# Kernel tuning notes

Measured on AMD Instinct MI355X. Metric: run time of the kernel, lower is better.

## Reference

```python
import jax, jax.numpy as jnp
import numpy as np

DIM = 512
HEADS = 8
HEAD_DIM = DIM // HEADS
HIDDEN = 4 * DIM
EPS = 1e-5


def _ln(x, g, b):
    mu = jnp.mean(x, axis=-1, keepdims=True)
    var = jnp.mean((x - mu) ** 2, axis=-1, keepdims=True)
    return (x - mu) * jax.lax.rsqrt(var + EPS) * g + b


def setup_inputs() -> dict:
    key = jax.random.key(0)
    ks = jax.random.split(key, 12)
    s = lambda fan: 1.0 / np.sqrt(fan)
    return {
        "x": jax.random.normal(ks[0], (2, 4096, DIM), jnp.float32),
        "ln1_g": jnp.ones((DIM,), jnp.float32),
        "ln1_b": jnp.zeros((DIM,), jnp.float32),
        "ln2_g": jnp.ones((DIM,), jnp.float32),
        "ln2_b": jnp.zeros((DIM,), jnp.float32),
        "qkv_w": jax.random.normal(ks[1], (3 * DIM, DIM), jnp.float32) * s(DIM),
        "qkv_b": jnp.zeros((3 * DIM,), jnp.float32),
        "proj_w": jax.random.normal(ks[2], (DIM, DIM), jnp.float32) * s(DIM),
        "proj_b": jnp.zeros((DIM,), jnp.float32),
        "fc1_w": jax.random.normal(ks[3], (HIDDEN, DIM), jnp.float32) * s(DIM),
        "fc1_b": jnp.zeros((HIDDEN,), jnp.float32),
        "fc2_w": jax.random.normal(ks[4], (DIM, HIDDEN), jnp.float32) * s(HIDDEN),
        "fc2_b": jnp.zeros((DIM,), jnp.float32),
    }


def reference(x, ln1_g, ln1_b, ln2_g, ln2_b, qkv_w, qkv_b, proj_w, proj_b,
              fc1_w, fc1_b, fc2_w, fc2_b):
    B, N, C = x.shape
    # --- attention (pre-norm) ---
    h = _ln(x, ln1_g, ln1_b)
    qkv = h @ qkv_w.T + qkv_b                      # [B,N,3C]
    qkv = qkv.reshape(B, N, 3, HEADS, HEAD_DIM)
    q, k, v = (jnp.moveaxis(qkv, 2, 0)[i].transpose(0, 2, 1, 3) for i in range(3))  # [B,H,N,D]
    scale = HEAD_DIM ** -0.5
    attn = jax.nn.softmax(jnp.einsum('bhnd,bhmd->bhnm', q, k) * scale, axis=-1)
    out = jnp.einsum('bhnm,bhmd->bhnd', attn, v)   # [B,H,N,D]
    out = out.transpose(0, 2, 1, 3).reshape(B, N, C)
    x = x + out @ proj_w.T + proj_b
    # --- MLP (pre-norm) ---
    h = _ln(x, ln2_g, ln2_b)
    h = jax.nn.gelu(h @ fc1_w.T + fc1_b, approximate=False)
    return x + h @ fc2_w.T + fc2_b
```

## Files before the change

kernel.cpp:

```cpp
#include <hip/hip_runtime.h>
#include <hip/hip_bf16.h>
#include <string.h>

using bf16 = __hip_bfloat16;
typedef __attribute__((ext_vector_type(8))) short short8;
typedef __attribute__((ext_vector_type(4))) float f32x4;
typedef __attribute__((ext_vector_type(16))) float f32x16;

#define GAS __attribute__((address_space(1)))
#define LAS __attribute__((address_space(3)))

__device__ __forceinline__ void gld_lds16(const void* g, void* l) {
  __builtin_amdgcn_global_load_lds((const GAS void*)g, (LAS void*)l, 16, 0, 0);
}

__device__ __forceinline__ unsigned short f2bfu(float f) {
  bf16 h = __float2bfloat16(f);
  return *reinterpret_cast<unsigned short*>(&h);
}

__device__ __forceinline__ unsigned pack_bf16x2(float lo, float hi) {
  __hip_bfloat162 v = __float22bfloat162_rn(make_float2(lo, hi));
  unsigned u;
  __builtin_memcpy(&u, &v, 4);
  return u;
}

__global__ __launch_bounds__(256) void cvt_all(const float* __restrict__ w0, bf16* __restrict__ o0,
                                               const float* __restrict__ w1, bf16* __restrict__ o1,
                                               const float* __restrict__ w2, bf16* __restrict__ o2,
                                               const float* __restrict__ w3, bf16* __restrict__ o3) {
  int i = blockIdx.x * 256 + threadIdx.x;
  const float* src; bf16* dst; int off;
  if (i < 196608)      { src = w0; dst = o0; off = i; }
  else if (i < 262144) { src = w1; dst = o1; off = i - 196608; }
  else if (i < 524288) { src = w2; dst = o2; off = i - 262144; }
  else                 { src = w3; dst = o3; off = i - 524288; }
  float4 v = reinterpret_cast<const float4*>(src)[off];
  ushort4 o;
  o.x = f2bfu(v.x); o.y = f2bfu(v.y); o.z = f2bfu(v.z); o.w = f2bfu(v.w);
  reinterpret_cast<ushort4*>(dst)[off] = o;
}

__global__ __launch_bounds__(256) void ln_kernel(const float* __restrict__ x,
                                                 const float* __restrict__ g,
                                                 const float* __restrict__ b,
                                                 bf16* __restrict__ out) {
  const int row = blockIdx.x * 4 + (threadIdx.x >> 6);
  const int lane = threadIdx.x & 63;
  const float4* xr = reinterpret_cast<const float4*>(x + (size_t)row * 512);
  float4 v0 = xr[lane], v1 = xr[64 + lane];
  float s  = v0.x + v0.y + v0.z + v0.w + v1.x + v1.y + v1.z + v1.w;
  float s2 = v0.x*v0.x + v0.y*v0.y + v0.z*v0.z + v0.w*v0.w
           + v1.x*v1.x + v1.y*v1.y + v1.z*v1.z + v1.w*v1.w;
  #pragma unroll
  for (int d = 1; d < 64; d <<= 1) { s += __shfl_xor(s, d); s2 += __shfl_xor(s2, d); }
  const float mu = s * (1.0f / 512.0f);
  const float var = s2 * (1.0f / 512.0f) - mu * mu;
  const float rstd = rsqrtf(var + 1e-5f);
  const float4* g4 = reinterpret_cast<const float4*>(g);
  const float4* b4 = reinterpret_cast<const float4*>(b);
  float4 ga = g4[lane], gb = g4[64 + lane], ba = b4[lane], bb = b4[64 + lane];
  ushort4 o0, o1;
  o0.x = f2bfu((v0.x - mu) * rstd * ga.x + ba.x);
  o0.y = f2bfu((v0.y - mu) * rstd * ga.y + ba.y);
  o0.z = f2bfu((v0.z - mu) * rstd * ga.z + ba.z);
  o0.w = f2bfu((v0.w - mu) * rstd * ga.w + ba.w);
  o1.x = f2bfu((v1.x - mu) * rstd * gb.x + bb.x);
  o1.y = f2bfu((v1.y - mu) * rstd * gb.y + bb.y);
  o1.z = f2bfu((v1.z - mu) * rstd * gb.z + bb.z);
  o1.w = f2bfu((v1.w - mu) * rstd * gb.w + bb.w);
  ushort4* orow = reinterpret_cast<ushort4*>(out + (size_t)row * 512);
  orow[lane] = o0;
  orow[64 + lane] = o1;
}

template <int EPI>
__global__ __launch_bounds__(256) void gemm_bt(const bf16* __restrict__ A,
                                               const bf16* __restrict__ B,
                                               const float* __restrict__ bias,
                                               const float* __restrict__ resid,
                                               void* __restrict__ Cv,
                                               int M, int N, int K) {
  __shared__ bf16 As[128 * 32];
  __shared__ bf16 Bs[128 * 32];
  const int tid = threadIdx.x;
  const int lane = tid & 63, wid = tid >> 6;
  const int lr = lane & 15, lg = lane >> 4;
  const int row0 = blockIdx.x * 128, col0 = blockIdx.y * 128;
  const int wr = (wid >> 1) * 64, wc = (wid & 1) * 64;
  f32x4 acc[4][4] = {};
  const int r1 = tid >> 2,          c1 = (tid & 3) * 8;
  const int r2 = (256 + tid) >> 2,  c2 = ((256 + tid) & 3) * 8;
  for (int kt = 0; kt < K; kt += 32) {
    __syncthreads();
    gld_lds16(A + (size_t)(row0 + r1) * K + kt + c1, As + tid * 8);
    gld_lds16(A + (size_t)(row0 + r2) * K + kt + c2, As + (256 + tid) * 8);
    gld_lds16(B + (size_t)(col0 + r1) * K + kt + c1, Bs + tid * 8);
    gld_lds16(B + (size_t)(col0 + r2) * K + kt + c2, Bs + (256 + tid) * 8);
    __syncthreads();
    short8 af[4], bfr[4];
    #pragma unroll
    for (int mi = 0; mi < 4; ++mi)
      af[mi] = *reinterpret_cast<const short8*>(&As[(wr + mi * 16 + lr) * 32 + lg * 8]);
    #pragma unroll
    for (int nj = 0; nj < 4; ++nj)
      bfr[nj] = *reinterpret_cast<const short8*>(&Bs[(wc + nj * 16 + lr) * 32 + lg * 8]);
    #pragma unroll
    for (int mi = 0; mi < 4; ++mi)
      #pragma unroll
      for (int nj = 0; nj < 4; ++nj)
        acc[mi][nj] = __builtin_amdgcn_mfma_f32_16x16x32_bf16(af[mi], bfr[nj], acc[mi][nj], 0, 0, 0);
  }
  #pragma unroll
  for (int mi = 0; mi < 4; ++mi) {
    #pragma unroll
    for (int nj = 0; nj < 4; ++nj) {
      const int col = col0 + wc + nj * 16 + lr;
      const float bv = bias ? bias[col] : 0.0f;
      #pragma unroll
      for (int rg = 0; rg < 4; ++rg) {
        const int row = row0 + wr + mi * 16 + lg * 4 + rg;
        float v = acc[mi][nj][rg] + bv;
        if constexpr (EPI == 1) v = 0.5f * v * (1.0f + erff(v * 0.70710678118654752f));
        if constexpr (EPI == 2) {
          reinterpret_cast<float*>(Cv)[(size_t)row * N + col] = v + resid[(size_t)row * N + col];
        } else {
          reinterpret_cast<bf16*>(Cv)[(size_t)row * N + col] = __float2bfloat16(v);
        }
      }
    }
  }
}

template <int EPI>
__global__ __launch_bounds__(256) void gemm_bt64(const bf16* __restrict__ A,
                                                 const bf16* __restrict__ B,
                                                 const float* __restrict__ bias,
                                                 const float* __restrict__ resid,
                                                 void* __restrict__ Cv,
                                                 int M, int N, int K) {
  __shared__ bf16 As[64 * 64];
  __shared__ bf16 Bs[64 * 64];
  const int tid = threadIdx.x;
  const int lane = tid & 63, wid = tid >> 6;
  const int lr = lane & 15, lg = lane >> 4;
  const int row0 = blockIdx.x * 64, col0 = blockIdx.y * 64;
  const int wr = (wid >> 1) * 32, wc = (wid & 1) * 32;
  f32x4 acc[2][2] = {};
  const int xsw = (lr & 7) << 4;
  const int fb0 = lr * 128 + ((lg * 16) ^ xsw);
  const int fb1 = lr * 128 + ((64 + lg * 16) ^ xsw);
  const int ph0 = tid * 16, ph1 = (256 + tid) * 16;
  const int r0 = ph0 >> 7, r1 = ph1 >> 7;
  const int lb0 = ph0 ^ ((r0 & 7) << 4), lb1 = ph1 ^ ((r1 & 7) << 4);
  const char* Ab0 = (const char*)A + (size_t)(row0 + r0) * K * 2 + (lb0 & 127);
  const char* Ab1 = (const char*)A + (size_t)(row0 + r1) * K * 2 + (lb1 & 127);
  const char* Bb0 = (const char*)B + (size_t)(col0 + r0) * K * 2 + (lb0 & 127);
  const char* Bb1 = (const char*)B + (size_t)(col0 + r1) * K * 2 + (lb1 & 127);
  for (int kt = 0; kt < K; kt += 64) {
    __syncthreads();
    gld_lds16(Ab0 + kt * 2, (char*)As + ph0);
    gld_lds16(Ab1 + kt * 2, (char*)As + ph1);
    gld_lds16(Bb0 + kt * 2, (char*)Bs + ph0);
    gld_lds16(Bb1 + kt * 2, (char*)Bs + ph1);
    __syncthreads();
    short8 af0[2], af1[2], bf0[2], bf1[2];
    #pragma unroll
    for (int mi = 0; mi < 2; ++mi) {
      af0[mi] = *reinterpret_cast<const short8*>((const char*)As + (wr + mi * 16) * 128 + fb0);
      af1[mi] = *reinterpret_cast<const short8*>((const char*)As + (wr + mi * 16) * 128 + fb1);
    }
    #pragma unroll
    for (int nj = 0; nj < 2; ++nj) {
      bf0[nj] = *reinterpret_cast<const short8*>((const char*)Bs + (wc + nj * 16) * 128 + fb0);
      bf1[nj] = *reinterpret_cast<const short8*>((const char*)Bs + (wc + nj * 16) * 128 + fb1);
    }
    #pragma unroll
    for (int mi = 0; mi < 2; ++mi)
      #pragma unroll
      for (int nj = 0; nj < 2; ++nj) {
        acc[mi][nj] = __builtin_amdgcn_mfma_f32_16x16x32_bf16(af0[mi], bf0[nj], acc[mi][nj], 0, 0, 0);
        acc[mi][nj] = __builtin_amdgcn_mfma_f32_16x16x32_bf16(af1[mi], bf1[nj], acc[mi][nj], 0, 0, 0);
      }
  }
  #pragma unroll
  for (int mi = 0; mi < 2; ++mi) {
    #pragma unroll
    for (int nj = 0; nj < 2; ++nj) {
      const int col = col0 + wc + nj * 16 + lr;
      const float bv = bias ? bias[col] : 0.0f;
      #pragma unroll
      for (int rg = 0; rg < 4; ++rg) {
        const int row = row0 + wr + mi * 16 + lg * 4 + rg;
        float v = acc[mi][nj][rg] + bv;
        if constexpr (EPI == 1) v = 0.5f * v * (1.0f + erff(v * 0.70710678118654752f));
        if constexpr (EPI == 2) {
          reinterpret_cast<float*>(Cv)[(size_t)row * N + col] = v + resid[(size_t)row * N + col];
        } else {
          reinterpret_cast<bf16*>(Cv)[(size_t)row * N + col] = __float2bfloat16(v);
        }
      }
    }
  }
}

__global__ __launch_bounds__(256) void reshape_qkv(const bf16* __restrict__ C,
                                                   bf16* __restrict__ q,
                                                   bf16* __restrict__ k,
                                                   bf16* __restrict__ vf) {
  const int nt = blockIdx.x;
  const int bh = blockIdx.y;
  const int b = bh >> 3, h = bh & 7;
  __shared__ alignas(16) bf16 vs[64][72];
  const int tid = threadIdx.x;
  const float qs = 0.125f * 1.44269504088896340736f;
  #pragma unroll
  for (int i = 0; i < 16; ++i) {
    const int idx = i * 256 + tid;
    const int rr = idx >> 6, c = idx & 63;
    const size_t crow = ((size_t)b * 4096 + nt * 64 + rr) * 1536;
    const size_t onb = ((size_t)bh * 4096 + nt * 64 + rr) * 64 + c;
    q[onb] = __float2bfloat16(__bfloat162float(C[crow + h * 64 + c]) * qs);
    k[onb] = C[crow + 512 + h * 64 + c];
    vs[c][rr] = C[crow + 1024 + h * 64 + c];
  }
  __syncthreads();
  #pragma unroll
  for (int i = 0; i < 2; ++i) {
    const int s = i * 256 + tid;
    const int half = (s >> 8) & 1, db = (s >> 7) & 1, c = (s >> 6) & 1, l = s & 63;
    const int d = db * 32 + (l & 31);
    const int n0 = half * 32 + c * 16 + ((l >> 5) << 2);
    const short4 lo = *reinterpret_cast<const short4*>(&vs[d][n0]);
    const short4 hi = *reinterpret_cast<const short4*>(&vs[d][n0 + 8]);
    short8 v;
    v[0] = lo.x; v[1] = lo.y; v[2] = lo.z; v[3] = lo.w;
    v[4] = hi.x; v[5] = hi.y; v[6] = hi.z; v[7] = hi.w;
    bf16* dst = vf + ((size_t)bh * 128 + nt * 2 + half) * 2048 + (db * 2 + c) * 512 + (size_t)l * 8;
    *reinterpret_cast<short8*>(dst) = v;
  }
}

__global__ __launch_bounds__(256, 4) void attn_kernel(const bf16* __restrict__ Q,
                                                      const bf16* __restrict__ K,
                                                      const bf16* __restrict__ Vf,
                                                      bf16* __restrict__ Out) {
  const int qt = blockIdx.x;
  const int bh = blockIdx.y;
  const int b = bh >> 3, h = bh & 7;
  __shared__ alignas(16) char smem[17408];
  const int tid = threadIdx.x, w = tid >> 6, lane = tid & 63;
  const int qg = w >> 1, kvh = w & 1;
  const int l31 = lane & 31, hi = lane >> 5;

  const bf16* qrow = Q + ((size_t)bh * 4096 + qt * 64 + qg * 32 + l31) * 64 + hi * 8;
  const short8 qf0 = *reinterpret_cast<const short8*>(qrow);
  const short8 qf1 = *reinterpret_cast<const short8*>(qrow + 16);
  const short8 qf2 = *reinterpret_cast<const short8*>(qrow + 32);
  const short8 qf3 = *reinterpret_cast<const short8*>(qrow + 48);

  const char* KgB = (const char*)K + (size_t)bh * 524288;
  const int php = tid * 16;
  const int rowp = php >> 7;
  const int lbp = php ^ ((rowp & 7) << 4);
  const int xswl = (lane & 7) << 4;
  const int fk0 = l31 * 128 + (( 0 + hi * 16) ^ xswl);
  const int fk1 = l31 * 128 + ((32 + hi * 16) ^ xswl);
  const int fk2 = l31 * 128 + ((64 + hi * 16) ^ xswl);
  const int fk3 = l31 * 128 + ((96 + hi * 16) ^ xswl);
  const int kvh4096 = kvh * 4096;
  const char* vwp = (const char*)Vf + ((size_t)bh * 128 + (size_t)kvh * 64) * 4096 + lane * 16;

  f32x16 O0 = {}, O1 = {};
  float mrow = -1e30f, lrow = 0.0f;

  gld_lds16(KgB + lbp, smem + php);
  gld_lds16(KgB + 262144 + lbp, smem + 4096 + php);
  int koff = 4096;

  auto stage = [&](int buf) {
    gld_lds16(KgB + koff + lbp, smem + buf * 8192 + php);
    gld_lds16(KgB + 262144 + koff + lbp, smem + buf * 8192 + 4096 + php);
    koff += 4096;
  };

  auto compute = [&](int buf) {
    const short8 va00 = *reinterpret_cast<const short8*>(vwp);
    const short8 va01 = *reinterpret_cast<const short8*>(vwp + 1024);
    const short8 va10 = *reinterpret_cast<const short8*>(vwp + 2048);
    const short8 va11 = *reinterpret_cast<const short8*>(vwp + 3072);
    vwp += 4096;
    const char* kt = smem + buf * 8192 + kvh4096;
    const short8 kf0 = *reinterpret_cast<const short8*>(kt + fk0);
    const short8 kf1 = *reinterpret_cast<const short8*>(kt + fk1);
    const short8 kf2 = *reinterpret_cast<const short8*>(kt + fk2);
    const short8 kf3 = *reinterpret_cast<const short8*>(kt + fk3);
    f32x16 S = {};
    __builtin_amdgcn_s_setprio(1);
    S = __builtin_amdgcn_mfma_f32_32x32x16_bf16(kf0, qf0, S, 0, 0, 0);
    S = __builtin_amdgcn_mfma_f32_32x32x16_bf16(kf1, qf1, S, 0, 0, 0);
    S = __builtin_amdgcn_mfma_f32_32x32x16_bf16(kf2, qf2, S, 0, 0, 0);
    S = __builtin_amdgcn_mfma_f32_32x32x16_bf16(kf3, qf3, S, 0, 0, 0);
    __builtin_amdgcn_s_setprio(0);
    float a0 = fmaxf(fmaxf(S[0], S[1]), fmaxf(S[2], S[3]));
    float a1 = fmaxf(fmaxf(S[4], S[5]), fmaxf(S[6], S[7]));
    float a2 = fmaxf(fmaxf(S[8], S[9]), fmaxf(S[10], S[11]));
    float a3 = fmaxf(fmaxf(S[12], S[13]), fmaxf(S[14], S[15]));
    float rmax = fmaxf(fmaxf(a0, a1), fmaxf(a2, a3));
    float ra = rmax, rb = rmax;
    asm volatile("v_permlane32_swap_b32 %0, %1" : "+v"(ra), "+v"(rb));
    rmax = fmaxf(ra, rb);
    if (!__all(rmax <= mrow + 8.0f)) {
      const float mnew = fmaxf(mrow, rmax);
      const float fsc = __builtin_amdgcn_exp2f(mrow - mnew);
      lrow *= fsc;
      #pragma unroll
      for (int i = 0; i < 16; ++i) { O0[i] *= fsc; O1[i] *= fsc; }
      mrow = mnew;
    }
    #pragma unroll
    for (int i = 0; i < 16; ++i) S[i] = __builtin_amdgcn_exp2f(S[i] - mrow);
    float s0 = (S[0] + S[1]) + (S[2] + S[3]);
    float s1 = (S[4] + S[5]) + (S[6] + S[7]);
    float s2 = (S[8] + S[9]) + (S[10] + S[11]);
    float s3 = (S[12] + S[13]) + (S[14] + S[15]);
    float rsum = (s0 + s1) + (s2 + s3);
    float sa = rsum, sb = rsum;
    asm volatile("v_permlane32_swap_b32 %0, %1" : "+v"(sa), "+v"(sb));
    lrow += sa + sb;
    union U8 { unsigned u[4]; short8 s8; };
    __builtin_amdgcn_s_setprio(1);
    {
      U8 ph, pl;
      ph.u[0] = pack_bf16x2(S[0], S[1]);  ph.u[1] = pack_bf16x2(S[2], S[3]);
      ph.u[2] = pack_bf16x2(S[4], S[5]);  ph.u[3] = pack_bf16x2(S[6], S[7]);
      float lo[8];
      #pragma unroll
      for (int e = 0; e < 8; ++e) {
        unsigned hv = (e & 1) ? (ph.u[e >> 1] & 0xFFFF0000u) : (ph.u[e >> 1] << 16);
        float hf; __builtin_memcpy(&hf, &hv, 4);
        lo[e] = S[e] - hf;
      }
      pl.u[0] = pack_bf16x2(lo[0], lo[1]); pl.u[1] = pack_bf16x2(lo[2], lo[3]);
      pl.u[2] = pack_bf16x2(lo[4], lo[5]); pl.u[3] = pack_bf16x2(lo[6], lo[7]);
      O0 = __builtin_amdgcn_mfma_f32_32x32x16_bf16(va00, ph.s8, O0, 0, 0, 0);
      O0 = __builtin_amdgcn_mfma_f32_32x32x16_bf16(va00, pl.s8, O0, 0, 0, 0);
      O1 = __builtin_amdgcn_mfma_f32_32x32x16_bf16(va10, ph.s8, O1, 0, 0, 0);
      O1 = __builtin_amdgcn_mfma_f32_32x32x16_bf16(va10, pl.s8, O1, 0, 0, 0);
    }
    {
      U8 ph, pl;
      ph.u[0] = pack_bf16x2(S[8], S[9]);   ph.u[1] = pack_bf16x2(S[10], S[11]);
      ph.u[2] = pack_bf16x2(S[12], S[13]); ph.u[3] = pack_bf16x2(S[14], S[15]);
      float lo[8];
      #pragma unroll
      for (int e = 0; e < 8; ++e) {
        unsigned hv = (e & 1) ? (ph.u[e >> 1] & 0xFFFF0000u) : (ph.u[e >> 1] << 16);
        float hf; __builtin_memcpy(&hf, &hv, 4);
        lo[e] = S[8 + e] - hf;
      }
      pl.u[0] = pack_bf16x2(lo[0], lo[1]); pl.u[1] = pack_bf16x2(lo[2], lo[3]);
      pl.u[2] = pack_bf16x2(lo[4], lo[5]); pl.u[3] = pack_bf16x2(lo[6], lo[7]);
      O0 = __builtin_amdgcn_mfma_f32_32x32x16_bf16(va01, ph.s8, O0, 0, 0, 0);
      O0 = __builtin_amdgcn_mfma_f32_32x32x16_bf16(va01, pl.s8, O0, 0, 0, 0);
      O1 = __builtin_amdgcn_mfma_f32_32x32x16_bf16(va11, ph.s8, O1, 0, 0, 0);
      O1 = __builtin_amdgcn_mfma_f32_32x32x16_bf16(va11, pl.s8, O1, 0, 0, 0);
    }
    __builtin_amdgcn_s_setprio(0);
  };

  for (int tt = 0; tt < 31; ++tt) {
    __syncthreads(); stage(1); compute(0);
    __syncthreads(); stage(0); compute(1);
  }
  __syncthreads(); stage(1); compute(0);
  __syncthreads(); compute(1);

  __syncthreads();
  float* area = reinterpret_cast<float*>(smem) + qg * 2176;
  if (kvh) {
    #pragma unroll
    for (int r = 0; r < 16; ++r) {
      area[r * 64 + lane] = O0[r];
      area[(16 + r) * 64 + lane] = O1[r];
    }
    area[2048 + lane] = mrow;
    area[2112 + lane] = lrow;
  }
  __syncthreads();
  if (!kvh) {
    const float mB = area[2048 + lane], lB = area[2112 + lane];
    const float mx = fmaxf(mrow, mB);
    const float fa = __builtin_amdgcn_exp2f(mrow - mx);
    const float fb = __builtin_amdgcn_exp2f(mB - mx);
    const float inv = 1.0f / (lrow * fa + lB * fb);
    const int qrow = qt * 64 + qg * 32 + l31;
    bf16* ob = Out + ((size_t)b * 4096 + qrow) * 512 + h * 64 + hi * 4;
    #pragma unroll
    for (int db = 0; db < 2; ++db) {
      #pragma unroll
      for (int rq = 0; rq < 4; ++rq) {
        const int r = rq * 4;
        float v0 = ((db ? O1[r + 0] : O0[r + 0]) * fa + area[(db * 16 + r + 0) * 64 + lane] * fb) * inv;
        float v1 = ((db ? O1[r + 1] : O0[r + 1]) * fa + area[(db * 16 + r + 1) * 64 + lane] * fb) * inv;
        float v2 = ((db ? O1[r + 2] : O0[r + 2]) * fa + area[(db * 16 + r + 2) * 64 + lane] * fb) * inv;
        float v3 = ((db ? O1[r + 3] : O0[r + 3]) * fa + area[(db * 16 + r + 3) * 64 + lane] * fb) * inv;
        uint2 st;
        st.x = pack_bf16x2(v0, v1);
        st.y = pack_bf16x2(v2, v3);
        *reinterpret_cast<uint2*>(ob + db * 32 + rq * 8) = st;
      }
    }
  }
}

extern "C" void kernel_launch(void* const* d_in, const int* in_sizes, int n_in,
                              void* d_out, int out_size, void* d_ws, size_t ws_size,
                              hipStream_t stream) {
  const float* x      = (const float*)d_in[0];
  const float* ln1_g  = (const float*)d_in[1];
  const float* ln1_b  = (const float*)d_in[2];
  const float* ln2_g  = (const float*)d_in[3];
  const float* ln2_b  = (const float*)d_in[4];
  const float* qkv_w  = (const float*)d_in[5];
  const float* qkv_b  = (const float*)d_in[6];
  const float* proj_w = (const float*)d_in[7];
  const float* proj_b = (const float*)d_in[8];
  const float* fc1_w  = (const float*)d_in[9];
  const float* fc1_b  = (const float*)d_in[10];
  const float* fc2_w  = (const float*)d_in[11];
  const float* fc2_b  = (const float*)d_in[12];

  char* ws = (char*)d_ws;
  constexpr size_t o_qkvw = 0;
  constexpr size_t o_projw = 1572864;
  constexpr size_t o_fc1w  = 2097152;
  constexpr size_t o_fc2w  = 4194304;
  constexpr size_t o_h     = 6291456;
  constexpr size_t o_qkvC  = 14680064;
  constexpr size_t o_q     = 39845888;
  constexpr size_t o_k     = 48234496;
  constexpr size_t o_vt    = 56623104;
  constexpr size_t o_attn  = 65011712;
  constexpr size_t o_x2    = 73400320;
  constexpr size_t o_fc1o  = o_qkvC;
  constexpr size_t needed  = 90177536;
  if (ws_size < needed) return;

  bf16* qkvw_bf = (bf16*)(ws + o_qkvw);
  bf16* projw_bf = (bf16*)(ws + o_projw);
  bf16* fc1w_bf = (bf16*)(ws + o_fc1w);
  bf16* fc2w_bf = (bf16*)(ws + o_fc2w);
  bf16* h    = (bf16*)(ws + o_h);
  bf16* qkvC = (bf16*)(ws + o_qkvC);
  bf16* q    = (bf16*)(ws + o_q);
  bf16* k    = (bf16*)(ws + o_k);
  bf16* vf   = (bf16*)(ws + o_vt);
  bf16* attn = (bf16*)(ws + o_attn);
  float* x2  = (float*)(ws + o_x2);
  bf16* fc1o = (bf16*)(ws + o_fc1o);
  float* out = (float*)d_out;

  cvt_all<<<3072, 256, 0, stream>>>(qkv_w, qkvw_bf, proj_w, projw_bf, fc1_w, fc1w_bf, fc2_w, fc2w_bf);

  ln_kernel<<<2048, 256, 0, stream>>>(x, ln1_g, ln1_b, h);
  gemm_bt<0><<<dim3(64, 12), 256, 0, stream>>>(h, qkvw_bf, qkv_b, nullptr, qkvC, 8192, 1536, 512);
  reshape_qkv<<<dim3(64, 16), 256, 0, stream>>>(qkvC, q, k, vf);
  attn_kernel<<<dim3(64, 16), 256, 0, stream>>>(q, k, vf, attn);
  gemm_bt64<2><<<dim3(128, 8), 256, 0, stream>>>(attn, projw_bf, proj_b, x, x2, 8192, 512, 512);
  ln_kernel<<<2048, 256, 0, stream>>>(x2, ln2_g, ln2_b, h);
  gemm_bt<1><<<dim3(64, 16), 256, 0, stream>>>(h, fc1w_bf, fc1_b, nullptr, fc1o, 8192, 2048, 512);
  gemm_bt64<2><<<dim3(128, 8), 256, 0, stream>>>(fc1o, fc2w_bf, fc2_b, x2, out, 8192, 512, 2048);
}
```

Measured before the change: 279.3 us.

## Switch attention path to fp16 with pre-swizzled K and drop split-bf16 P·V

The QKV GEMM now writes fp16 output. The reshape kernel emits Q, plus K and V both in an MFMA-fragment-ordered layout. The attention kernel uses f16 MFMAs and packs P once into fp16, replacing the bf16 hi/lo split that needed two MFMAs per P·V product. The LDS double-buffered K staging with per-tile barriers is removed, and K fragments are read straight from global memory like V. This halves the P·V MFMA count and drops the barriers, at the cost of fp16 range limits and K reads that are no longer shared through LDS.

```diff
diff --git a/kernel.cpp b/kernel.cpp
--- a/kernel.cpp
+++ b/kernel.cpp
@@ -1,9 +1,11 @@
 #include <hip/hip_runtime.h>
 #include <hip/hip_bf16.h>
+#include <hip/hip_fp16.h>
 #include <string.h>
 
 using bf16 = __hip_bfloat16;
 typedef __attribute__((ext_vector_type(8))) short short8;
+typedef __attribute__((ext_vector_type(8))) _Float16 half8;
 typedef __attribute__((ext_vector_type(4))) float f32x4;
 typedef __attribute__((ext_vector_type(16))) float f32x16;
 
@@ -21,6 +23,13 @@
 
 __device__ __forceinline__ unsigned pack_bf16x2(float lo, float hi) {
   __hip_bfloat162 v = __float22bfloat162_rn(make_float2(lo, hi));
+  unsigned u;
+  __builtin_memcpy(&u, &v, 4);
+  return u;
+}
+
+__device__ __forceinline__ unsigned pack_f16x2(float lo, float hi) {
+  __half2 v = __float22half2_rn(make_float2(lo, hi));
   unsigned u;
   __builtin_memcpy(&u, &v, 4);
   return u;
@@ -125,6 +134,8 @@
         if constexpr (EPI == 1) v = 0.5f * v * (1.0f + erff(v * 0.70710678118654752f));
         if constexpr (EPI == 2) {
           reinterpret_cast<float*>(Cv)[(size_t)row * N + col] = v + resid[(size_t)row * N + col];
+        } else if constexpr (EPI == 3) {
+          reinterpret_cast<__half*>(Cv)[(size_t)row * N + col] = __float2half(v);
         } else {
           reinterpret_cast<bf16*>(Cv)[(size_t)row * N + col] = __float2bfloat16(v);
         }
@@ -205,14 +216,14 @@
   }
 }
 
-__global__ __launch_bounds__(256) void reshape_qkv(const bf16* __restrict__ C,
-                                                   bf16* __restrict__ q,
-                                                   bf16* __restrict__ k,
-                                                   bf16* __restrict__ vf) {
+__global__ __launch_bounds__(256) void reshape_qkv(const __half* __restrict__ C,
+                                                   __half* __restrict__ q,
+                                                   __half* __restrict__ KF,
+                                                   __half* __restrict__ VF) {
   const int nt = blockIdx.x;
   const int bh = blockIdx.y;
   const int b = bh >> 3, h = bh & 7;
-  __shared__ alignas(16) bf16 vs[64][72];
+  __shared__ alignas(16) __half vs[64][72];
   const int tid = threadIdx.x;
   const float qs = 0.125f * 1.44269504088896340736f;
   #pragma unroll
@@ -221,30 +232,39 @@
     const int rr = idx >> 6, c = idx & 63;
     const size_t crow = ((size_t)b * 4096 + nt * 64 + rr) * 1536;
     const size_t onb = ((size_t)bh * 4096 + nt * 64 + rr) * 64 + c;
-    q[onb] = __float2bfloat16(__bfloat162float(C[crow + h * 64 + c]) * qs);
-    k[onb] = C[crow + 512 + h * 64 + c];
+    q[onb] = __float2half(__half2float(C[crow + h * 64 + c]) * qs);
     vs[c][rr] = C[crow + 1024 + h * 64 + c];
   }
-  __syncthreads();
   #pragma unroll
   for (int i = 0; i < 2; ++i) {
     const int s = i * 256 + tid;
-    const int half = (s >> 8) & 1, db = (s >> 7) & 1, c = (s >> 6) & 1, l = s & 63;
+    const int half_ = s >> 8, dc = (s >> 6) & 3, l = s & 63;
+    const int l31 = l & 31, hi2 = l >> 5;
+    const __half* src = C + ((size_t)b * 4096 + nt * 64 + half_ * 32 + l31) * 1536
+                          + 512 + h * 64 + dc * 16 + hi2 * 8;
+    __half* dst = KF + ((size_t)bh * 128 + nt * 2 + half_) * 2048 + dc * 512 + (size_t)l * 8;
+    *reinterpret_cast<short8*>(dst) = *reinterpret_cast<const short8*>(src);
+  }
+  __syncthreads();
+  #pragma unroll
+  for (int i = 0; i < 2; ++i) {
+    const int s = i * 256 + tid;
+    const int half_ = (s >> 8) & 1, db = (s >> 7) & 1, c = (s >> 6) & 1, l = s & 63;
     const int d = db * 32 + (l & 31);
-    const int n0 = half * 32 + c * 16 + ((l >> 5) << 2);
+    const int n0 = half_ * 32 + c * 16 + ((l >> 5) << 2);
     const short4 lo = *reinterpret_cast<const short4*>(&vs[d][n0]);
     const short4 hi = *reinterpret_cast<const short4*>(&vs[d][n0 + 8]);
     short8 v;
     v[0] = lo.x; v[1] = lo.y; v[2] = lo.z; v[3] = lo.w;
     v[4] = hi.x; v[5] = hi.y; v[6] = hi.z; v[7] = hi.w;
-    bf16* dst = vf + ((size_t)bh * 128 + nt * 2 + half) * 2048 + (db * 2 + c) * 512 + (size_t)l * 8;
+    __half* dst = VF + ((size_t)bh * 128 + nt * 2 + half_) * 2048 + (db * 2 + c) * 512 + (size_t)l * 8;
     *reinterpret_cast<short8*>(dst) = v;
   }
 }
 
-__global__ __launch_bounds__(256, 4) void attn_kernel(const bf16* __restrict__ Q,
-                                                      const bf16* __restrict__ K,
-                                                      const bf16* __restrict__ Vf,
+__global__ __launch_bounds__(256, 4) void attn_kernel(const __half* __restrict__ Q,
+                                                      const __half* __restrict__ KF,
+                                                      const __half* __restrict__ VF,
                                                       bf16* __restrict__ Out) {
   const int qt = blockIdx.x;
   const int bh = blockIdx.y;
@@ -254,54 +274,35 @@
   const int qg = w >> 1, kvh = w & 1;
   const int l31 = lane & 31, hi = lane >> 5;
 
-  const bf16* qrow = Q + ((size_t)bh * 4096 + qt * 64 + qg * 32 + l31) * 64 + hi * 8;
-  const short8 qf0 = *reinterpret_cast<const short8*>(qrow);
-  const short8 qf1 = *reinterpret_cast<const short8*>(qrow + 16);
-  const short8 qf2 = *reinterpret_cast<const short8*>(qrow + 32);
-  const short8 qf3 = *reinterpret_cast<const short8*>(qrow + 48);
-
-  const char* KgB = (const char*)K + (size_t)bh * 524288;
-  const int php = tid * 16;
-  const int rowp = php >> 7;
-  const int lbp = php ^ ((rowp & 7) << 4);
-  const int xswl = (lane & 7) << 4;
-  const int fk0 = l31 * 128 + (( 0 + hi * 16) ^ xswl);
-  const int fk1 = l31 * 128 + ((32 + hi * 16) ^ xswl);
-  const int fk2 = l31 * 128 + ((64 + hi * 16) ^ xswl);
-  const int fk3 = l31 * 128 + ((96 + hi * 16) ^ xswl);
-  const int kvh4096 = kvh * 4096;
-  const char* vwp = (const char*)Vf + ((size_t)bh * 128 + (size_t)kvh * 64) * 4096 + lane * 16;
+  const __half* qrow = Q + ((size_t)bh * 4096 + qt * 64 + qg * 32 + l31) * 64 + hi * 8;
+  const half8 qf0 = *reinterpret_cast<const half8*>(qrow);
+  const half8 qf1 = *reinterpret_cast<const half8*>(qrow + 16);
+  const half8 qf2 = *reinterpret_cast<const half8*>(qrow + 32);
+  const half8 qf3 = *reinterpret_cast<const half8*>(qrow + 48);
+
+  const char* kfp = (const char*)KF + (size_t)bh * 524288 + (size_t)kvh * 262144 + lane * 16;
+  const char* vfp = (const char*)VF + (size_t)bh * 524288 + (size_t)kvh * 262144 + lane * 16;
 
   f32x16 O0 = {}, O1 = {};
   float mrow = -1e30f, lrow = 0.0f;
 
-  gld_lds16(KgB + lbp, smem + php);
-  gld_lds16(KgB + 262144 + lbp, smem + 4096 + php);
-  int koff = 4096;
-
-  auto stage = [&](int buf) {
-    gld_lds16(KgB + koff + lbp, smem + buf * 8192 + php);
-    gld_lds16(KgB + 262144 + koff + lbp, smem + buf * 8192 + 4096 + php);
-    koff += 4096;
-  };
-
-  auto compute = [&](int buf) {
-    const short8 va00 = *reinterpret_cast<const short8*>(vwp);
-    const short8 va01 = *reinterpret_cast<const short8*>(vwp + 1024);
-    const short8 va10 = *reinterpret_cast<const short8*>(vwp + 2048);
-    const short8 va11 = *reinterpret_cast<const short8*>(vwp + 3072);
-    vwp += 4096;
-    const char* kt = smem + buf * 8192 + kvh4096;
-    const short8 kf0 = *reinterpret_cast<const short8*>(kt + fk0);
-    const short8 kf1 = *reinterpret_cast<const short8*>(kt + fk1);
-    const short8 kf2 = *reinterpret_cast<const short8*>(kt + fk2);
-    const short8 kf3 = *reinterpret_cast<const short8*>(kt + fk3);
+  for (int t = 0; t < 64; ++t) {
+    const half8 va00 = *reinterpret_cast<const half8*>(vfp);
+    const half8 va01 = *reinterpret_cast<const half8*>(vfp + 1024);
+    const half8 va10 = *reinterpret_cast<const half8*>(vfp + 2048);
+    const half8 va11 = *reinterpret_cast<const half8*>(vfp + 3072);
+    vfp += 4096;
+    const half8 kf0 = *reinterpret_cast<const half8*>(kfp);
+    const half8 kf1 = *reinterpret_cast<const half8*>(kfp + 1024);
+    const half8 kf2 = *reinterpret_cast<const half8*>(kfp + 2048);
+    const half8 kf3 = *reinterpret_cast<const half8*>(kfp + 3072);
+    kfp += 4096;
     f32x16 S = {};
     __builtin_amdgcn_s_setprio(1);
-    S = __builtin_amdgcn_mfma_f32_32x32x16_bf16(kf0, qf0, S, 0, 0, 0);
-    S = __builtin_amdgcn_mfma_f32_32x32x16_bf16(kf1, qf1, S, 0, 0, 0);
-    S = __builtin_amdgcn_mfma_f32_32x32x16_bf16(kf2, qf2, S, 0, 0, 0);
-    S = __builtin_amdgcn_mfma_f32_32x32x16_bf16(kf3, qf3, S, 0, 0, 0);
+    S = __builtin_amdgcn_mfma_f32_32x32x16_f16(kf0, qf0, S, 0, 0, 0);
+    S = __builtin_amdgcn_mfma_f32_32x32x16_f16(kf1, qf1, S, 0, 0, 0);
+    S = __builtin_amdgcn_mfma_f32_32x32x16_f16(kf2, qf2, S, 0, 0, 0);
+    S = __builtin_amdgcn_mfma_f32_32x32x16_f16(kf3, qf3, S, 0, 0, 0);
     __builtin_amdgcn_s_setprio(0);
     float a0 = fmaxf(fmaxf(S[0], S[1]), fmaxf(S[2], S[3]));
     float a1 = fmaxf(fmaxf(S[4], S[5]), fmaxf(S[6], S[7]));
@@ -329,53 +330,18 @@
     float sa = rsum, sb = rsum;
     asm volatile("v_permlane32_swap_b32 %0, %1" : "+v"(sa), "+v"(sb));
     lrow += sa + sb;
-    union U8 { unsigned u[4]; short8 s8; };
+    union U8 { unsigned u[4]; half8 h8; } up0, up1;
+    up0.u[0] = pack_f16x2(S[0], S[1]);   up0.u[1] = pack_f16x2(S[2], S[3]);
+    up0.u[2] = pack_f16x2(S[4], S[5]);   up0.u[3] = pack_f16x2(S[6], S[7]);
+    up1.u[0] = pack_f16x2(S[8], S[9]);   up1.u[1] = pack_f16x2(S[10], S[11]);
+    up1.u[2] = pack_f16x2(S[12], S[13]); up1.u[3] = pack_f16x2(S[14], S[15]);
     __builtin_amdgcn_s_setprio(1);
-    {
-      U8 ph, pl;
-      ph.u[0] = pack_bf16x2(S[0], S[1]);  ph.u[1] = pack_bf16x2(S[2], S[3]);
-      ph.u[2] = pack_bf16x2(S[4], S[5]);  ph.u[3] = pack_bf16x2(S[6], S[7]);
-      float lo[8];
-      #pragma unroll
-      for (int e = 0; e < 8; ++e) {
-        unsigned hv = (e & 1) ? (ph.u[e >> 1] & 0xFFFF0000u) : (ph.u[e >> 1] << 16);
-        float hf; __builtin_memcpy(&hf, &hv, 4);
-        lo[e] = S[e] - hf;
-      }
-      pl.u[0] = pack_bf16x2(lo[0], lo[1]); pl.u[1] = pack_bf16x2(lo[2], lo[3]);
-      pl.u[2] = pack_bf16x2(lo[4], lo[5]); pl.u[3] = pack_bf16x2(lo[6], lo[7]);
-      O0 = __builtin_amdgcn_mfma_f32_32x32x16_bf16(va00, ph.s8, O0, 0, 0, 0);
-      O0 = __builtin_amdgcn_mfma_f32_32x32x16_bf16(va00, pl.s8, O0, 0, 0, 0);
-      O1 = __builtin_amdgcn_mfma_f32_32x32x16_bf16(va10, ph.s8, O1, 0, 0, 0);
-      O1 = __builtin_amdgcn_mfma_f32_32x32x16_bf16(va10, pl.s8, O1, 0, 0, 0);
-    }
-    {
-      U8 ph, pl;
-      ph.u[0] = pack_bf16x2(S[8], S[9]);   ph.u[1] = pack_bf16x2(S[10], S[11]);
-      ph.u[2] = pack_bf16x2(S[12], S[13]); ph.u[3] = pack_bf16x2(S[14], S[15]);
-      float lo[8];
-      #pragma unroll
-      for (int e = 0; e < 8; ++e) {
-        unsigned hv = (e & 1) ? (ph.u[e >> 1] & 0xFFFF0000u) : (ph.u[e >> 1] << 16);
-        float hf; __builtin_memcpy(&hf, &hv, 4);
-        lo[e] = S[8 + e] - hf;
-      }
-      pl.u[0] = pack_bf16x2(lo[0], lo[1]); pl.u[1] = pack_bf16x2(lo[2], lo[3]);
-      pl.u[2] = pack_bf16x2(lo[4], lo[5]); pl.u[3] = pack_bf16x2(lo[6], lo[7]);
-      O0 = __builtin_amdgcn_mfma_f32_32x32x16_bf16(va01, ph.s8, O0, 0, 0, 0);
-      O0 = __builtin_amdgcn_mfma_f32_32x32x16_bf16(va01, pl.s8, O0, 0, 0, 0);
-      O1 = __builtin_amdgcn_mfma_f32_32x32x16_bf16(va11, ph.s8, O1, 0, 0, 0);
-      O1 = __builtin_amdgcn_mfma_f32_32x32x16_bf16(va11, pl.s8, O1, 0, 0, 0);
-    }
+    O0 = __builtin_amdgcn_mfma_f32_32x32x16_f16(va00, up0.h8, O0, 0, 0, 0);
+    O0 = __builtin_amdgcn_mfma_f32_32x32x16_f16(va01, up1.h8, O0, 0, 0, 0);
+    O1 = __builtin_amdgcn_mfma_f32_32x32x16_f16(va10, up0.h8, O1, 0, 0, 0);
+    O1 = __builtin_amdgcn_mfma_f32_32x32x16_f16(va11, up1.h8, O1, 0, 0, 0);
     __builtin_amdgcn_s_setprio(0);
-  };
-
-  for (int tt = 0; tt < 31; ++tt) {
-    __syncthreads(); stage(1); compute(0);
-    __syncthreads(); stage(0); compute(1);
-  }
-  __syncthreads(); stage(1); compute(0);
-  __syncthreads(); compute(1);
+  }
 
   __syncthreads();
   float* area = reinterpret_cast<float*>(smem) + qg * 2176;
@@ -395,8 +361,8 @@
     const float fa = __builtin_amdgcn_exp2f(mrow - mx);
     const float fb = __builtin_amdgcn_exp2f(mB - mx);
     const float inv = 1.0f / (lrow * fa + lB * fb);
-    const int qrow = qt * 64 + qg * 32 + l31;
-    bf16* ob = Out + ((size_t)b * 4096 + qrow) * 512 + h * 64 + hi * 4;
+    const int qrow2 = qt * 64 + qg * 32 + l31;
+    bf16* ob = Out + ((size_t)b * 4096 + qrow2) * 512 + h * 64 + hi * 4;
     #pragma unroll
     for (int db = 0; db < 2; ++db) {
       #pragma unroll
@@ -452,22 +418,22 @@
   bf16* projw_bf = (bf16*)(ws + o_projw);
   bf16* fc1w_bf = (bf16*)(ws + o_fc1w);
   bf16* fc2w_bf = (bf16*)(ws + o_fc2w);
-  bf16* h    = (bf16*)(ws + o_h);
-  bf16* qkvC = (bf16*)(ws + o_qkvC);
-  bf16* q    = (bf16*)(ws + o_q);
-  bf16* k    = (bf16*)(ws + o_k);
-  bf16* vf   = (bf16*)(ws + o_vt);
-  bf16* attn = (bf16*)(ws + o_attn);
-  float* x2  = (float*)(ws + o_x2);
-  bf16* fc1o = (bf16*)(ws + o_fc1o);
-  float* out = (float*)d_out;
+  bf16* h     = (bf16*)(ws + o_h);
+  __half* qkvC = (__half*)(ws + o_qkvC);
+  __half* q    = (__half*)(ws + o_q);
+  __half* kf   = (__half*)(ws + o_k);
+  __half* vf   = (__half*)(ws + o_vt);
+  bf16* attn  = (bf16*)(ws + o_attn);
+  float* x2   = (float*)(ws + o_x2);
+  bf16* fc1o  = (bf16*)(ws + o_fc1o);
+  float* out  = (float*)d_out;
 
   cvt_all<<<3072, 256, 0, stream>>>(qkv_w, qkvw_bf, proj_w, projw_bf, fc1_w, fc1w_bf, fc2_w, fc2w_bf);
 
   ln_kernel<<<2048, 256, 0, stream>>>(x, ln1_g, ln1_b, h);
-  gemm_bt<0><<<dim3(64, 12), 256, 0, stream>>>(h, qkvw_bf, qkv_b, nullptr, qkvC, 8192, 1536, 512);
-  reshape_qkv<<<dim3(64, 16), 256, 0, stream>>>(qkvC, q, k, vf);
-  attn_kernel<<<dim3(64, 16), 256, 0, stream>>>(q, k, vf, attn);
+  gemm_bt<3><<<dim3(64, 12), 256, 0, stream>>>(h, qkvw_bf, qkv_b, nullptr, qkvC, 8192, 1536, 512);
+  reshape_qkv<<<dim3(64, 16), 256, 0, stream>>>(qkvC, q, kf, vf);
+  attn_kernel<<<dim3(64, 16), 256, 0, stream>>>(q, kf, vf, attn);
   gemm_bt64<2><<<dim3(128, 8), 256, 0, stream>>>(attn, projw_bf, proj_b, x, x2, 8192, 512, 512);
   ln_kernel<<<2048, 256, 0, stream>>>(x2, ln2_g, ln2_b, h);
   gemm_bt<1><<<dim3(64, 16), 256, 0, stream>>>(h, fc1w_bf, fc1_b, nullptr, fc1o, 8192, 2048, 512);
```

After: 251.2 us. 10.1% less time.
